# Performance work log

Measured on AMD Instinct MI355X. Metric: run time of the kernel, lower is better.

Reference implementation:

```python
import jax, jax.numpy as jnp
import numpy as np

B, S, D = 2, 2048, 2048
H = 16
HD = D // H  # head_dim = 128


def setup_inputs() -> dict:
    key = jax.random.key(0)
    ks = jax.random.split(key, 5)
    scale = 1.0 / np.sqrt(D)
    x = jax.random.normal(ks[0], (B, S, D), dtype=jnp.float32)
    Wq = jax.random.normal(ks[1], (D, D), dtype=jnp.float32) * scale
    Wk = jax.random.normal(ks[2], (D, D), dtype=jnp.float32) * scale
    Wv = jax.random.normal(ks[3], (D, D), dtype=jnp.float32) * scale
    Wo = jax.random.normal(ks[4], (D, D), dtype=jnp.float32) * scale
    bo = jnp.zeros((D,), dtype=jnp.float32)
    return {"x": x, "Wq": Wq, "Wk": Wk, "Wv": Wv, "Wo": Wo, "bo": bo}


def reference(x, Wq, Wk, Wv, Wo, bo):
    b, s, _ = x.shape
    # projections (nn.Linear: y = x @ W^T, here W stored as [in, out] already)
    q = (x @ Wq).reshape(b, s, H, HD).transpose(0, 2, 1, 3)  # [B,H,S,HD]
    k = (x @ Wk).reshape(b, s, H, HD).transpose(0, 2, 1, 3)
    v = (x @ Wv).reshape(b, s, H, HD).transpose(0, 2, 1, 3)
    scores = jnp.einsum("bhqd,bhkd->bhqk", q, k)
    causal = jnp.triu(jnp.ones((s, s), dtype=bool), k=1)
    scores = jnp.where(causal[None, None], -jnp.inf, scores)
    attn = jax.nn.softmax(scores / np.sqrt(HD), axis=-1)  # dropout=0 (eval)
    out = jnp.einsum("bhqk,bhkd->bhqd", attn, v)
    out = out.transpose(0, 2, 1, 3).reshape(b, s, D)
    return out @ Wo + bo
```

## Files before the change

### kernel.cpp

```cpp
#include <hip/hip_runtime.h>

#define S_LEN 2048
#define D_MODEL 2048
#define NH 16
#define HD 128

typedef __attribute__((ext_vector_type(4))) float f32x4;
typedef __attribute__((ext_vector_type(8))) short short8;
typedef __attribute__((ext_vector_type(8))) __bf16 bf16x8;
typedef __attribute__((ext_vector_type(4))) unsigned short us4;

__device__ __forceinline__ unsigned short f2bf(float f) {
  unsigned int u = __builtin_bit_cast(unsigned int, f);
  return (unsigned short)((u + 0x7fffu + ((u >> 16) & 1u)) >> 16);
}

__device__ __forceinline__ f32x4 mfma_bf16(short8 a, short8 b, f32x4 c) {
  return __builtin_amdgcn_mfma_f32_16x16x32_bf16(
      __builtin_bit_cast(bf16x8, a), __builtin_bit_cast(bf16x8, b), c, 0, 0, 0);
}

__device__ __forceinline__ void gload16(const unsigned short* g, unsigned short* l) {
  __builtin_amdgcn_global_load_lds(
      (const __attribute__((address_space(1))) void*)g,
      (__attribute__((address_space(3))) void*)l, 16, 0, 0);
}

__global__ void cast_bf16_2(const float* __restrict__ src, unsigned short* __restrict__ dst0,
                            unsigned short* __restrict__ dst1) {
  int i = blockIdx.x * blockDim.x + threadIdx.x;
  float4 v = ((const float4*)src)[i];
  us4 o = { f2bf(v.x), f2bf(v.y), f2bf(v.z), f2bf(v.w) };
  if (i < 1048576) ((us4*)dst0)[i] = o;
  else             ((us4*)dst1)[i - 1048576] = o;
}

__global__ void transpose_cast3(const float* __restrict__ Wq, const float* __restrict__ Wk,
                                const float* __restrict__ Wv, unsigned short* __restrict__ Wt) {
  __shared__ unsigned short tile[32][33];
  const float* W = (blockIdx.z == 0) ? Wq : (blockIdx.z == 1) ? Wk : Wv;
  unsigned short* dst = Wt + (size_t)blockIdx.z * 4194304;
  int bx = blockIdx.x * 32, by = blockIdx.y * 32;
  int tx = threadIdx.x, ty = threadIdx.y;
#pragma unroll
  for (int i = 0; i < 32; i += 8)
    tile[ty + i][tx] = f2bf(W[(by + ty + i) * D_MODEL + bx + tx]);
  __syncthreads();
#pragma unroll
  for (int i = 0; i < 32; i += 8)
    dst[(bx + ty + i) * D_MODEL + by + tx] = tile[tx][ty + i];
}

__global__ void transpose_cast(const float* __restrict__ W, unsigned short* __restrict__ Wt) {
  __shared__ unsigned short tile[32][33];
  int bx = blockIdx.x * 32, by = blockIdx.y * 32;
  int tx = threadIdx.x, ty = threadIdx.y;
#pragma unroll
  for (int i = 0; i < 32; i += 8)
    tile[ty + i][tx] = f2bf(W[(by + ty + i) * D_MODEL + bx + tx]);
  __syncthreads();
#pragma unroll
  for (int i = 0; i < 32; i += 8)
    Wt[(bx + ty + i) * D_MODEL + by + tx] = tile[tx][ty + i];
}

#define GEMM_KLOOP(Ag0, Ag1, Bg0, Bg1, acc, t, fu, wr, wc, lr)           \
  __shared__ unsigned short lA[3][128 * 32];                             \
  __shared__ unsigned short lB[3][128 * 32];                             \
  do {                                                                   \
    const int nt = D_MODEL >> 5;                                         \
    _Pragma("unroll") for (int i = 0; i < 2; i++) {                      \
      const int _k = i * 32;                                             \
      gload16(Ag0 + _k, lA[i] + t * 8);                                  \
      gload16(Ag1 + _k, lA[i] + 2048 + t * 8);                           \
      gload16(Bg0 + _k, lB[i] + t * 8);                                  \
      gload16(Bg1 + _k, lB[i] + 2048 + t * 8);                           \
    }                                                                    \
    int cur = 0;                                                         \
    for (int tk = 0; tk < nt; ++tk) {                                    \
      if (tk + 1 < nt) {                                                 \
        asm volatile("s_waitcnt vmcnt(4)" ::: "memory");                 \
      } else {                                                           \
        asm volatile("s_waitcnt vmcnt(0)" ::: "memory");                 \
      }                                                                  \
      __builtin_amdgcn_sched_barrier(0);                                 \
      __builtin_amdgcn_s_barrier();                                      \
      __builtin_amdgcn_sched_barrier(0);                                 \
      if (tk + 2 < nt) {                                                 \
        int nx2 = cur + 2;                                               \
        if (nx2 >= 3) nx2 -= 3;                                          \
        const int _k = (tk + 2) * 32;                                    \
        gload16(Ag0 + _k, lA[nx2] + t * 8);                              \
        gload16(Ag1 + _k, lA[nx2] + 2048 + t * 8);                       \
        gload16(Bg0 + _k, lB[nx2] + t * 8);                              \
        gload16(Bg1 + _k, lB[nx2] + 2048 + t * 8);                       \
      }                                                                  \
      const unsigned short* a = lA[cur];                                 \
      const unsigned short* b = lB[cur];                                 \
      short8 af[4], bf[4];                                               \
      _Pragma("unroll") for (int mi = 0; mi < 4; mi++)                   \
        af[mi] = *(const short8*)&a[(wr * 64 + mi * 16 + lr) * 32 + fu]; \
      _Pragma("unroll") for (int ni = 0; ni < 4; ni++)                   \
        bf[ni] = *(const short8*)&b[(wc * 64 + ni * 16 + lr) * 32 + fu]; \
      __builtin_amdgcn_s_setprio(1);                                     \
      _Pragma("unroll") for (int mi = 0; mi < 4; mi++)                   \
        _Pragma("unroll") for (int ni = 0; ni < 4; ni++)                 \
          acc[mi][ni] = mfma_bf16(af[mi], bf[ni], acc[mi][ni]);          \
      __builtin_amdgcn_s_setprio(0);                                     \
      cur = (cur == 2) ? 0 : cur + 1;                                    \
    }                                                                    \
  } while (0)

__global__ __launch_bounds__(256, 3) void gemm_qkv(
    const unsigned short* __restrict__ A, const unsigned short* __restrict__ Bt,
    unsigned short* __restrict__ qb, unsigned short* __restrict__ kb,
    unsigned short* __restrict__ vtb) {
  const int t = threadIdx.x;
  const int l = t & 63, w = t >> 6;
  const int wr = w >> 1, wc = w & 1;
  const int lr = l & 15, lk = l >> 4;
  const int n0 = blockIdx.x * 128, m0 = blockIdx.y * 128;

  const int arow = t >> 2;
  const int au = ((t & 3) ^ ((arow >> 1) & 3)) * 8;
  const unsigned short* Ag0 = A + (size_t)(m0 + arow) * D_MODEL + au;
  const unsigned short* Ag1 = Ag0 + 64 * D_MODEL;
  const unsigned short* Bg0 = Bt + (size_t)(n0 + arow) * D_MODEL + au;
  const unsigned short* Bg1 = Bg0 + 64 * D_MODEL;
  const int fu = (lk ^ ((lr >> 1) & 3)) * 8;

  f32x4 acc[4][4] = {};
  GEMM_KLOOP(Ag0, Ag1, Bg0, Bg1, acc, t, fu, wr, wc, lr);

  if (n0 < 4096) {
    unsigned short* C = (n0 < 2048) ? qb : kb;
    const int nbase = n0 & 2047;
#pragma unroll
    for (int mi = 0; mi < 4; mi++) {
      int r0 = m0 + wr * 64 + mi * 16 + lk * 4;
#pragma unroll
      for (int ni = 0; ni < 4; ni++) {
        int c2 = nbase + wc * 64 + ni * 16 + lr;
#pragma unroll
        for (int r = 0; r < 4; r++)
          C[(size_t)(r0 + r) * D_MODEL + c2] = f2bf(acc[mi][ni][r]);
      }
    }
  } else {
    const int nb = n0 - 4096;
#pragma unroll
    for (int mi = 0; mi < 4; mi++) {
      int s = m0 + wr * 64 + mi * 16 + lk * 4;
#pragma unroll
      for (int ni = 0; ni < 4; ni++) {
        int n = nb + wc * 64 + ni * 16 + lr;
        int h = n >> 7, d = n & (HD - 1);
        us4 pk = { f2bf(acc[mi][ni][0]), f2bf(acc[mi][ni][1]),
                   f2bf(acc[mi][ni][2]), f2bf(acc[mi][ni][3]) };
        *(us4*)&vtb[((size_t)(h * HD + d)) * S_LEN + s] = pk;
      }
    }
  }
}

__global__ __launch_bounds__(256, 3) void gemm_out(
    const unsigned short* __restrict__ ctx0, const unsigned short* __restrict__ ctx1,
    const unsigned short* __restrict__ Bt, const float* __restrict__ bias,
    float* __restrict__ out) {
  const int t = threadIdx.x;
  const int l = t & 63, w = t >> 6;
  const int wr = w >> 1, wc = w & 1;
  const int lr = l & 15, lk = l >> 4;
  const int n0 = blockIdx.x * 128, m0 = blockIdx.y * 128;

  const unsigned short* Ablk = (m0 < 2048)
      ? ctx0 + (size_t)m0 * D_MODEL
      : ctx1 + (size_t)(m0 - 2048) * D_MODEL;

  const int arow = t >> 2;
  const int au = ((t & 3) ^ ((arow >> 1) & 3)) * 8;
  const unsigned short* Ag0 = Ablk + (size_t)arow * D_MODEL + au;
  const unsigned short* Ag1 = Ag0 + 64 * D_MODEL;
  const unsigned short* Bg0 = Bt + (size_t)(n0 + arow) * D_MODEL + au;
  const unsigned short* Bg1 = Bg0 + 64 * D_MODEL;
  const int fu = (lk ^ ((lr >> 1) & 3)) * 8;

  f32x4 acc[4][4] = {};
  GEMM_KLOOP(Ag0, Ag1, Bg0, Bg1, acc, t, fu, wr, wc, lr);

#pragma unroll
  for (int mi = 0; mi < 4; mi++) {
    int r0 = m0 + wr * 64 + mi * 16 + lk * 4;
#pragma unroll
    for (int ni = 0; ni < 4; ni++) {
      int c2 = n0 + wc * 64 + ni * 16 + lr;
      float bv = bias[c2];
#pragma unroll
      for (int r = 0; r < 4; r++)
        out[(size_t)(r0 + r) * D_MODEL + c2] = acc[mi][ni][r] + bv;
    }
  }
}

__global__ __launch_bounds__(256, 2) void attn_kernel(
    const unsigned short* __restrict__ Q, const unsigned short* __restrict__ K,
    const unsigned short* __restrict__ Vt, unsigned short* __restrict__ ctx) {
  __shared__ unsigned short lds[36864];

  const int id = blockIdx.x;
  const int h = id & 15;
  const int qtl = id >> 4;
  const int qt = (qtl < 16) ? (2 * qtl) : (63 - 2 * qtl);

  const int t = threadIdx.x, l = t & 63, w = t >> 6;
  const int lr = l & 15, lk = l >> 4;

  const float qscale = 0.08838834764831845f * 1.44269504088896340f;
  const unsigned short* qsrc = Q + (size_t)(qt * 64 + w * 16 + lr) * D_MODEL + h * HD;
  short8 Qf[4];
#pragma unroll
  for (int kk = 0; kk < 4; kk++) {
    short8 qv = *(const short8*)&qsrc[kk * 32 + lk * 8];
#pragma unroll
    for (int e = 0; e < 8; e++) {
      unsigned int u = ((unsigned int)(unsigned short)qv[e]) << 16;
      float f = __builtin_bit_cast(float, u) * qscale;
      qv[e] = (short)f2bf(f);
    }
    Qf[kk] = qv;
  }

  const unsigned short* ksrc = K + h * HD;
  const unsigned short* vsrc = Vt + (size_t)h * HD * S_LEN;
  const int krow = t >> 4, kcs = t & 15;
  const int vrow = t >> 3, vcs = t & 7;

#define STAGE_KV(par, kv0base)                                                    \
  do {                                                                            \
    unsigned short* lKb = lds + (par) * 8192;                                     \
    unsigned short* lVb = lds + 16384 + (par) * 8192;                             \
    _Pragma("unroll") for (int i = 0; i < 4; i++) {                               \
      int row = i * 16 + krow;                                                    \
      gload16(ksrc + (size_t)((kv0base) + row) * D_MODEL + ((kcs ^ (row & 7)) * 8), \
              lKb + row * 128 + kcs * 8);                                         \
    }                                                                             \
    _Pragma("unroll") for (int i = 0; i < 4; i++) {                               \
      int row = i * 32 + vrow;                                                    \
      gload16(vsrc + (size_t)row * S_LEN + (kv0base) + ((vcs ^ (row & 7)) * 8),   \
              lVb + row * 64 + vcs * 8);                                          \
    }                                                                             \
  } while (0)

  f32x4 O[8] = {};
  float l_s = 0.f;
  const float M0 = 8.0f;
  const int nkv = qt + 1;
  unsigned short* lPw = lds + 32768 + w * 1024;

  STAGE_KV(0, 0);

  for (int tk = 0; tk < nkv; tk++) {
    const int kv0 = tk * 64;
    const int par = tk & 1;
    const unsigned short* lKc = lds + par * 8192;
    const unsigned short* lVc = lds + 16384 + par * 8192;

    asm volatile("s_waitcnt vmcnt(0)" ::: "memory");
    __builtin_amdgcn_sched_barrier(0);
    __builtin_amdgcn_s_barrier();
    __builtin_amdgcn_sched_barrier(0);

    if (tk + 1 < nkv) STAGE_KV(par ^ 1, kv0 + 64);

    f32x4 sc[4] = {};
    __builtin_amdgcn_s_setprio(1);
#pragma unroll
    for (int kk = 0; kk < 4; kk++) {
      short8 Kf[4];
#pragma unroll
      for (int ni = 0; ni < 4; ni++)
        Kf[ni] = *(const short8*)&lKc[(ni * 16 + lr) * 128 + (((kk * 4 + lk) ^ (lr & 7)) * 8)];
#pragma unroll
      for (int ni = 0; ni < 4; ni++)
        sc[ni] = mfma_bf16(Kf[ni], Qf[kk], sc[ni]);
    }
    __builtin_amdgcn_s_setprio(0);

    const int row0g = qt * 64 + w * 16 + lr;
    if (tk == qt) {
#pragma unroll
      for (int ni = 0; ni < 4; ni++) {
        const int colb = kv0 + ni * 16 + lk * 4;
#pragma unroll
        for (int r = 0; r < 4; r++)
          if (colb + r > row0g) sc[ni][r] = -1e30f;
      }
    }

    float rs = 0.f;
#pragma unroll
    for (int ni = 0; ni < 4; ni++)
#pragma unroll
      for (int r = 0; r < 4; r++) {
        float p = __builtin_amdgcn_exp2f(sc[ni][r] - M0);
        sc[ni][r] = p;
        rs += p;
      }
    rs += __shfl_xor(rs, 16);
    rs += __shfl_xor(rs, 32);
    l_s += rs;

#pragma unroll
    for (int ni = 0; ni < 4; ni++) {
      us4 pk = { f2bf(sc[ni][0]), f2bf(sc[ni][1]), f2bf(sc[ni][2]), f2bf(sc[ni][3]) };
      int u16 = (ni * 2 + (lk >> 1)) ^ (lr & 7);
      *(us4*)&lPw[lr * 64 + u16 * 8 + (lk & 1) * 4] = pk;
    }

    __builtin_amdgcn_s_setprio(1);
#pragma unroll
    for (int kk = 0; kk < 2; kk++) {
      short8 Pf = *(const short8*)&lPw[lr * 64 + (((kk * 4 + lk) ^ (lr & 7)) * 8)];
#pragma unroll
      for (int di = 0; di < 8; di++) {
        short8 Vf = *(const short8*)&lVc[(di * 16 + lr) * 64 + (((kk * 4 + lk) ^ (lr & 7)) * 8)];
        O[di] = mfma_bf16(Pf, Vf, O[di]);
      }
    }
    __builtin_amdgcn_s_setprio(0);
  }
#undef STAGE_KV

  float lr4[4];
#pragma unroll
  for (int r = 0; r < 4; r++) lr4[r] = __shfl(l_s, lk * 4 + r);
#pragma unroll
  for (int di = 0; di < 8; di++)
#pragma unroll
    for (int r = 0; r < 4; r++) {
      float v = O[di][r] / lr4[r];
      ctx[(size_t)(qt * 64 + w * 16 + lk * 4 + r) * D_MODEL + h * HD + di * 16 + lr] = f2bf(v);
    }
}

extern "C" void kernel_launch(void* const* d_in, const int* in_sizes, int n_in,
                              void* d_out, int out_size, void* d_ws, size_t ws_size,
                              hipStream_t stream) {
  const float* x  = (const float*)d_in[0];
  const float* Wq = (const float*)d_in[1];
  const float* Wk = (const float*)d_in[2];
  const float* Wv = (const float*)d_in[3];
  const float* Wo = (const float*)d_in[4];
  const float* bo = (const float*)d_in[5];
  float* out = (float*)d_out;

  unsigned short* ws = (unsigned short*)d_ws;
  unsigned short* S0 = ws;
  unsigned short* S1 = ws + 1 * 4194304;
  unsigned short* S2 = ws + 2 * 4194304;
  unsigned short* S3 = ws + 3 * 4194304;
  unsigned short* S4 = ws + 4 * 4194304;
  unsigned short* wqkvt = (unsigned short*)d_out;
  unsigned short* xb1   = wqkvt + 12582912;

  dim3 tb(32, 8);

  transpose_cast3<<<dim3(64, 64, 3), tb, 0, stream>>>(Wq, Wk, Wv, wqkvt);
  cast_bf16_2<<<8192, 256, 0, stream>>>(x, S0, xb1);

  for (int b = 0; b < 2; b++) {
    const unsigned short* xb = (b == 0) ? S0 : xb1;
    unsigned short* ctx = (b == 0) ? S4 : S0;

    gemm_qkv<<<dim3(48, 16), 256, 0, stream>>>(xb, wqkvt, S1, S2, S3);
    attn_kernel<<<dim3(512), 256, 0, stream>>>(S1, S2, S3, ctx);
  }

  transpose_cast<<<dim3(64, 64), tb, 0, stream>>>(Wo, S1);
  gemm_out<<<dim3(16, 32), 256, 0, stream>>>(S4, S0, S1, bo, out);
}
```

Before: 284.5 us.

## Rewrite QKV GEMM as 256x256-tile 8-wave kernel with interleaved staging

Replaces the 128x128-tile, 4-wave QKV projection GEMM with a 256x256-tile, 512-thread kernel. It uses double-buffered LDS with 64-wide K steps and a hand-scheduled sequence of barriers that interleaves global-to-LDS loads with quarter-tile MFMA groups. The larger tile raises arithmetic intensity and cuts redundant global traffic. In exchange the grid shrinks to 192 blocks per batch, fewer than the CU count, and LDS use per block rises to about 128 KB, which limits occupancy to one block per CU.

```diff
diff --git a/kernel.cpp b/kernel.cpp
--- a/kernel.cpp
+++ b/kernel.cpp
@@ -62,6 +62,150 @@
 #pragma unroll
   for (int i = 0; i < 32; i += 8)
     Wt[(bx + ty + i) * D_MODEL + by + tx] = tile[tx][ty + i];
+}
+
+__global__ __launch_bounds__(512, 2) void gemm_qkv(
+    const unsigned short* __restrict__ A, const unsigned short* __restrict__ Bt,
+    unsigned short* __restrict__ qb, unsigned short* __restrict__ kb,
+    unsigned short* __restrict__ vtb) {
+  __shared__ unsigned short lA[2][16384];
+  __shared__ unsigned short lB[2][16384];
+  const int t = threadIdx.x;
+  const int l = t & 63, w = t >> 6;
+  const int wm = w >> 2, wn = w & 3;
+  const int lr = l & 15, lk = l >> 4;
+  const int n0 = blockIdx.x * 256, m0 = blockIdx.y * 256;
+
+  const int t8 = t * 8;
+  const int srow = t >> 3;
+  const int gu8 = ((t & 7) ^ ((t >> 3) & 7)) * 8;
+  const unsigned short* asrc = A + (size_t)(m0 + srow) * D_MODEL + gu8;
+  const unsigned short* bsrc = Bt + (size_t)(n0 + srow) * D_MODEL + gu8;
+
+  const int aBase = (wm * 128 + lr) * 64;
+  const int bBase = (wn * 64 + lr) * 64;
+  const int aoff0 = (lk ^ (lr & 7)) * 8;
+  const int aoff1 = ((4 + lk) ^ (lr & 7)) * 8;
+
+  f32x4 acc[8][4] = {};
+  short8 af[4][2], bf[4][2];
+
+#define STG_A8(buf, koff, j) gload16(asrc + (size_t)(j) * 131072 + (koff), lA[buf] + (j) * 4096 + t8)
+#define STG_B8(buf, koff, j) gload16(bsrc + (size_t)(j) * 131072 + (koff), lB[buf] + (j) * 4096 + t8)
+#define RDA(p, mi0)                                                          \
+  _Pragma("unroll") for (int m = 0; m < 4; m++) {                            \
+    af[m][0] = *(const short8*)&lA[p][aBase + ((mi0) + m) * 1024 + aoff0];   \
+    af[m][1] = *(const short8*)&lA[p][aBase + ((mi0) + m) * 1024 + aoff1];   \
+  }
+#define RDB(p, ni0)                                                          \
+  _Pragma("unroll") for (int n = 0; n < 2; n++) {                            \
+    bf[(ni0) + n][0] = *(const short8*)&lB[p][bBase + ((ni0) + n) * 1024 + aoff0]; \
+    bf[(ni0) + n][1] = *(const short8*)&lB[p][bBase + ((ni0) + n) * 1024 + aoff1]; \
+  }
+#define MM16(mi0, ni0)                                                       \
+  __builtin_amdgcn_s_setprio(1);                                             \
+  _Pragma("unroll") for (int m = 0; m < 4; m++)                              \
+  _Pragma("unroll") for (int n = 0; n < 2; n++) {                            \
+    acc[(mi0)+m][(ni0)+n] = mfma_bf16(af[m][0], bf[(ni0)+n][0], acc[(mi0)+m][(ni0)+n]); \
+    acc[(mi0)+m][(ni0)+n] = mfma_bf16(af[m][1], bf[(ni0)+n][1], acc[(mi0)+m][(ni0)+n]); \
+  }                                                                          \
+  __builtin_amdgcn_s_setprio(0);
+#define BARRIER asm volatile("s_barrier" ::: "memory")
+#define SCHED0 __builtin_amdgcn_sched_barrier(0)
+
+#pragma unroll
+  for (int j = 0; j < 4; j++) STG_A8(0, 0, j);
+#pragma unroll
+  for (int j = 0; j < 4; j++) STG_B8(0, 0, j);
+  STG_A8(1, 64, 0); STG_A8(1, 64, 1);
+  asm volatile("s_waitcnt vmcnt(2)" ::: "memory");
+  BARRIER;
+
+#pragma unroll 1
+  for (int i = 0; i < 16; ++i) {
+    const bool more = (i < 15);
+    const size_t o1 = (size_t)(2 * i + 1) * 64;
+    const size_t o2 = (size_t)(2 * i + 2) * 64;
+    const size_t o3 = (size_t)(2 * i + 3) * 64;
+    RDA(0, 0); RDB(0, 0);
+    STG_A8(1, o1, 2); STG_A8(1, o1, 3);
+    BARRIER; SCHED0;
+    MM16(0, 0);
+    BARRIER;
+    RDB(0, 2);
+    STG_B8(1, o1, 0); STG_B8(1, o1, 1);
+    BARRIER; SCHED0;
+    MM16(0, 2);
+    BARRIER;
+    RDA(0, 4);
+    STG_B8(1, o1, 2); STG_B8(1, o1, 3);
+    BARRIER; SCHED0;
+    MM16(4, 2);
+    BARRIER;
+    if (more) { STG_A8(0, o2, 0); STG_A8(0, o2, 1); }
+    BARRIER; SCHED0;
+    MM16(4, 0);
+    if (more) { asm volatile("s_waitcnt vmcnt(2)" ::: "memory"); }
+    else      { asm volatile("s_waitcnt vmcnt(0)" ::: "memory"); }
+    BARRIER;
+    RDA(1, 0); RDB(1, 0);
+    if (more) { STG_A8(0, o2, 2); STG_A8(0, o2, 3); }
+    BARRIER; SCHED0;
+    MM16(0, 0);
+    BARRIER;
+    RDB(1, 2);
+    if (more) { STG_B8(0, o2, 0); STG_B8(0, o2, 1); }
+    BARRIER; SCHED0;
+    MM16(0, 2);
+    BARRIER;
+    RDA(1, 4);
+    if (more) { STG_B8(0, o2, 2); STG_B8(0, o2, 3); }
+    BARRIER; SCHED0;
+    MM16(4, 2);
+    BARRIER;
+    if (more) { STG_A8(1, o3, 0); STG_A8(1, o3, 1); }
+    BARRIER; SCHED0;
+    MM16(4, 0);
+    if (more) { asm volatile("s_waitcnt vmcnt(2)" ::: "memory"); }
+    BARRIER;
+  }
+#undef STG_A8
+#undef STG_B8
+#undef RDA
+#undef RDB
+#undef MM16
+#undef BARRIER
+#undef SCHED0
+
+  if (n0 < 4096) {
+    unsigned short* C = (n0 < 2048) ? qb : kb;
+    const int nbase = n0 & 2047;
+#pragma unroll
+    for (int mi = 0; mi < 8; mi++) {
+      int r0 = m0 + wm * 128 + mi * 16 + lk * 4;
+#pragma unroll
+      for (int ni = 0; ni < 4; ni++) {
+        int c2 = nbase + wn * 64 + ni * 16 + lr;
+#pragma unroll
+        for (int r = 0; r < 4; r++)
+          C[(size_t)(r0 + r) * D_MODEL + c2] = f2bf(acc[mi][ni][r]);
+      }
+    }
+  } else {
+    const int nb0 = n0 - 4096;
+#pragma unroll
+    for (int mi = 0; mi < 8; mi++) {
+      int s = m0 + wm * 128 + mi * 16 + lk * 4;
+#pragma unroll
+      for (int ni = 0; ni < 4; ni++) {
+        int n = nb0 + wn * 64 + ni * 16 + lr;
+        int h = n >> 7, d = n & (HD - 1);
+        us4 pk = { f2bf(acc[mi][ni][0]), f2bf(acc[mi][ni][1]),
+                   f2bf(acc[mi][ni][2]), f2bf(acc[mi][ni][3]) };
+        *(us4*)&vtb[((size_t)(h * HD + d)) * S_LEN + s] = pk;
+      }
+    }
+  }
 }
 
 #define GEMM_KLOOP(Ag0, Ag1, Bg0, Bg1, acc, t, fu, wr, wc, lr)           \
@@ -111,58 +255,6 @@
     }                                                                    \
   } while (0)
 
-__global__ __launch_bounds__(256, 3) void gemm_qkv(
-    const unsigned short* __restrict__ A, const unsigned short* __restrict__ Bt,
-    unsigned short* __restrict__ qb, unsigned short* __restrict__ kb,
-    unsigned short* __restrict__ vtb) {
-  const int t = threadIdx.x;
-  const int l = t & 63, w = t >> 6;
-  const int wr = w >> 1, wc = w & 1;
-  const int lr = l & 15, lk = l >> 4;
-  const int n0 = blockIdx.x * 128, m0 = blockIdx.y * 128;
-
-  const int arow = t >> 2;
-  const int au = ((t & 3) ^ ((arow >> 1) & 3)) * 8;
-  const unsigned short* Ag0 = A + (size_t)(m0 + arow) * D_MODEL + au;
-  const unsigned short* Ag1 = Ag0 + 64 * D_MODEL;
-  const unsigned short* Bg0 = Bt + (size_t)(n0 + arow) * D_MODEL + au;
-  const unsigned short* Bg1 = Bg0 + 64 * D_MODEL;
-  const int fu = (lk ^ ((lr >> 1) & 3)) * 8;
-
-  f32x4 acc[4][4] = {};
-  GEMM_KLOOP(Ag0, Ag1, Bg0, Bg1, acc, t, fu, wr, wc, lr);
-
-  if (n0 < 4096) {
-    unsigned short* C = (n0 < 2048) ? qb : kb;
-    const int nbase = n0 & 2047;
-#pragma unroll
-    for (int mi = 0; mi < 4; mi++) {
-      int r0 = m0 + wr * 64 + mi * 16 + lk * 4;
-#pragma unroll
-      for (int ni = 0; ni < 4; ni++) {
-        int c2 = nbase + wc * 64 + ni * 16 + lr;
-#pragma unroll
-        for (int r = 0; r < 4; r++)
-          C[(size_t)(r0 + r) * D_MODEL + c2] = f2bf(acc[mi][ni][r]);
-      }
-    }
-  } else {
-    const int nb = n0 - 4096;
-#pragma unroll
-    for (int mi = 0; mi < 4; mi++) {
-      int s = m0 + wr * 64 + mi * 16 + lk * 4;
-#pragma unroll
-      for (int ni = 0; ni < 4; ni++) {
-        int n = nb + wc * 64 + ni * 16 + lr;
-        int h = n >> 7, d = n & (HD - 1);
-        us4 pk = { f2bf(acc[mi][ni][0]), f2bf(acc[mi][ni][1]),
-                   f2bf(acc[mi][ni][2]), f2bf(acc[mi][ni][3]) };
-        *(us4*)&vtb[((size_t)(h * HD + d)) * S_LEN + s] = pk;
-      }
-    }
-  }
-}
-
 __global__ __launch_bounds__(256, 3) void gemm_out(
     const unsigned short* __restrict__ ctx0, const unsigned short* __restrict__ ctx1,
     const unsigned short* __restrict__ Bt, const float* __restrict__ bias,
@@ -372,7 +464,7 @@
     const unsigned short* xb = (b == 0) ? S0 : xb1;
     unsigned short* ctx = (b == 0) ? S4 : S0;
 
-    gemm_qkv<<<dim3(48, 16), 256, 0, stream>>>(xb, wqkvt, S1, S2, S3);
+    gemm_qkv<<<dim3(24, 8), 512, 0, stream>>>(xb, wqkvt, S1, S2, S3);
     attn_kernel<<<dim3(512), 256, 0, stream>>>(S1, S2, S3, ctx);
   }
 
```

Result: no change. 289.8 us (+1.9%).

## Rewrite attention to load K/V directly into registers with split-KV waves

Applied to the files above, without the earlier changes.

The attention kernel drops LDS staging of K/V tiles and the per-wave P round-trip through shared memory. Each wave now loads 16-row K and V fragments straight from global memory into registers, double-buffered. The four waves split as two query groups by two interleaved KV halves, and the halves are merged through LDS at the end. P stays in registers and feeds a 16x16x16 MFMA, and the GEMM launch bounds occupancy hint drops from 3 to 2. This removes barriers and LDS traffic per KV tile, at the cost of uncoalesced global loads without cross-wave reuse, higher register pressure, and a final reduction step.

```diff
diff --git a/kernel.cpp b/kernel.cpp
--- a/kernel.cpp
+++ b/kernel.cpp
@@ -7,6 +7,7 @@
 
 typedef __attribute__((ext_vector_type(4))) float f32x4;
 typedef __attribute__((ext_vector_type(8))) short short8;
+typedef __attribute__((ext_vector_type(4))) short s16x4;
 typedef __attribute__((ext_vector_type(8))) __bf16 bf16x8;
 typedef __attribute__((ext_vector_type(4))) unsigned short us4;
 
@@ -18,6 +19,15 @@
 __device__ __forceinline__ f32x4 mfma_bf16(short8 a, short8 b, f32x4 c) {
   return __builtin_amdgcn_mfma_f32_16x16x32_bf16(
       __builtin_bit_cast(bf16x8, a), __builtin_bit_cast(bf16x8, b), c, 0, 0, 0);
+}
+
+__device__ __forceinline__ f32x4 mfma16_bf16(s16x4 a, s16x4 b, f32x4 c) {
+#if __has_builtin(__builtin_amdgcn_mfma_f32_16x16x16bf16_1k)
+  return __builtin_amdgcn_mfma_f32_16x16x16bf16_1k(a, b, c, 0, 0, 0);
+#else
+  asm("v_mfma_f32_16x16x16_bf16 %0, %1, %2, %0" : "+v"(c) : "v"(a), "v"(b));
+  return c;
+#endif
 }
 
 __device__ __forceinline__ void gload16(const unsigned short* g, unsigned short* l) {
@@ -111,7 +121,7 @@
     }                                                                    \
   } while (0)
 
-__global__ __launch_bounds__(256, 3) void gemm_qkv(
+__global__ __launch_bounds__(256, 2) void gemm_qkv(
     const unsigned short* __restrict__ A, const unsigned short* __restrict__ Bt,
     unsigned short* __restrict__ qb, unsigned short* __restrict__ kb,
     unsigned short* __restrict__ vtb) {
@@ -163,7 +173,7 @@
   }
 }
 
-__global__ __launch_bounds__(256, 3) void gemm_out(
+__global__ __launch_bounds__(256, 2) void gemm_out(
     const unsigned short* __restrict__ ctx0, const unsigned short* __restrict__ ctx1,
     const unsigned short* __restrict__ Bt, const float* __restrict__ bias,
     float* __restrict__ out) {
@@ -205,7 +215,8 @@
 __global__ __launch_bounds__(256, 2) void attn_kernel(
     const unsigned short* __restrict__ Q, const unsigned short* __restrict__ K,
     const unsigned short* __restrict__ Vt, unsigned short* __restrict__ ctx) {
-  __shared__ unsigned short lds[36864];
+  __shared__ float eO[2][16][64][4];
+  __shared__ float eL[2][2][16];
 
   const int id = blockIdx.x;
   const int h = id & 15;
@@ -213,134 +224,112 @@
   const int qt = (qtl < 16) ? (2 * qtl) : (63 - 2 * qtl);
 
   const int t = threadIdx.x, l = t & 63, w = t >> 6;
+  const int wq = w >> 1, wk = w & 1;
   const int lr = l & 15, lk = l >> 4;
+  const int qgb = qt * 64 + wq * 32;
 
   const float qscale = 0.08838834764831845f * 1.44269504088896340f;
-  const unsigned short* qsrc = Q + (size_t)(qt * 64 + w * 16 + lr) * D_MODEL + h * HD;
-  short8 Qf[4];
-#pragma unroll
-  for (int kk = 0; kk < 4; kk++) {
-    short8 qv = *(const short8*)&qsrc[kk * 32 + lk * 8];
-#pragma unroll
-    for (int e = 0; e < 8; e++) {
-      unsigned int u = ((unsigned int)(unsigned short)qv[e]) << 16;
-      float f = __builtin_bit_cast(float, u) * qscale;
-      qv[e] = (short)f2bf(f);
-    }
-    Qf[kk] = qv;
-  }
-
-  const unsigned short* ksrc = K + h * HD;
-  const unsigned short* vsrc = Vt + (size_t)h * HD * S_LEN;
-  const int krow = t >> 4, kcs = t & 15;
-  const int vrow = t >> 3, vcs = t & 7;
-
-#define STAGE_KV(par, kv0base)                                                    \
-  do {                                                                            \
-    unsigned short* lKb = lds + (par) * 8192;                                     \
-    unsigned short* lVb = lds + 16384 + (par) * 8192;                             \
-    _Pragma("unroll") for (int i = 0; i < 4; i++) {                               \
-      int row = i * 16 + krow;                                                    \
-      gload16(ksrc + (size_t)((kv0base) + row) * D_MODEL + ((kcs ^ (row & 7)) * 8), \
-              lKb + row * 128 + kcs * 8);                                         \
-    }                                                                             \
-    _Pragma("unroll") for (int i = 0; i < 4; i++) {                               \
-      int row = i * 32 + vrow;                                                    \
-      gload16(vsrc + (size_t)row * S_LEN + (kv0base) + ((vcs ^ (row & 7)) * 8),   \
-              lVb + row * 64 + vcs * 8);                                          \
-    }                                                                             \
+  short8 Qf[2][4];
+#pragma unroll
+  for (int qc = 0; qc < 2; qc++)
+#pragma unroll
+    for (int kk = 0; kk < 4; kk++) {
+      short8 qv = *(const short8*)&Q[(size_t)(qgb + qc * 16 + lr) * D_MODEL + h * HD + kk * 32 + lk * 8];
+#pragma unroll
+      for (int e = 0; e < 8; e++) {
+        unsigned int u = ((unsigned int)(unsigned short)qv[e]) << 16;
+        float f = __builtin_bit_cast(float, u) * qscale;
+        qv[e] = (short)f2bf(f);
+      }
+      Qf[qc][kk] = qv;
+    }
+
+  const unsigned short* kbase = K + h * HD;
+  const unsigned short* vbase = Vt + (size_t)h * HD * S_LEN;
+
+  const int nkv16 = qt * 4 + 2 + 2 * wq;
+  const int nt = (nkv16 - wk + 1) >> 1;
+
+  f32x4 O0[8] = {}, O1[8] = {};
+  float ls0 = 0.f, ls1 = 0.f;
+  short8 KA[4], KB[4];
+  s16x4 VA[8], VB[8];
+
+#define LOADKV(KX, VX, j_)                                                          \
+  do {                                                                              \
+    const int kv0_ = (wk + 2 * (j_)) * 16;                                          \
+    _Pragma("unroll") for (int kk = 0; kk < 4; kk++)                                \
+      KX[kk] = *(const short8*)&kbase[(size_t)(kv0_ + lr) * D_MODEL + kk * 32 + lk * 8]; \
+    _Pragma("unroll") for (int dt = 0; dt < 8; dt++)                                \
+      VX[dt] = *(const s16x4*)&vbase[(size_t)(dt * 16 + lr) * S_LEN + kv0_ + lk * 4];    \
   } while (0)
 
-  f32x4 O[8] = {};
-  float l_s = 0.f;
-  const float M0 = 8.0f;
-  const int nkv = qt + 1;
-  unsigned short* lPw = lds + 32768 + w * 1024;
-
-  STAGE_KV(0, 0);
-
-  for (int tk = 0; tk < nkv; tk++) {
-    const int kv0 = tk * 64;
-    const int par = tk & 1;
-    const unsigned short* lKc = lds + par * 8192;
-    const unsigned short* lVc = lds + 16384 + par * 8192;
-
-    asm volatile("s_waitcnt vmcnt(0)" ::: "memory");
-    __builtin_amdgcn_sched_barrier(0);
-    __builtin_amdgcn_s_barrier();
-    __builtin_amdgcn_sched_barrier(0);
-
-    if (tk + 1 < nkv) STAGE_KV(par ^ 1, kv0 + 64);
-
-    f32x4 sc[4] = {};
-    __builtin_amdgcn_s_setprio(1);
-#pragma unroll
-    for (int kk = 0; kk < 4; kk++) {
-      short8 Kf[4];
-#pragma unroll
-      for (int ni = 0; ni < 4; ni++)
-        Kf[ni] = *(const short8*)&lKc[(ni * 16 + lr) * 128 + (((kk * 4 + lk) ^ (lr & 7)) * 8)];
-#pragma unroll
-      for (int ni = 0; ni < 4; ni++)
-        sc[ni] = mfma_bf16(Kf[ni], Qf[kk], sc[ni]);
-    }
-    __builtin_amdgcn_s_setprio(0);
-
-    const int row0g = qt * 64 + w * 16 + lr;
-    if (tk == qt) {
-#pragma unroll
-      for (int ni = 0; ni < 4; ni++) {
-        const int colb = kv0 + ni * 16 + lk * 4;
-#pragma unroll
-        for (int r = 0; r < 4; r++)
-          if (colb + r > row0g) sc[ni][r] = -1e30f;
-      }
-    }
-
-    float rs = 0.f;
-#pragma unroll
-    for (int ni = 0; ni < 4; ni++)
-#pragma unroll
-      for (int r = 0; r < 4; r++) {
-        float p = __builtin_amdgcn_exp2f(sc[ni][r] - M0);
-        sc[ni][r] = p;
-        rs += p;
-      }
-    rs += __shfl_xor(rs, 16);
-    rs += __shfl_xor(rs, 32);
-    l_s += rs;
-
-#pragma unroll
-    for (int ni = 0; ni < 4; ni++) {
-      us4 pk = { f2bf(sc[ni][0]), f2bf(sc[ni][1]), f2bf(sc[ni][2]), f2bf(sc[ni][3]) };
-      int u16 = (ni * 2 + (lk >> 1)) ^ (lr & 7);
-      *(us4*)&lPw[lr * 64 + u16 * 8 + (lk & 1) * 4] = pk;
-    }
-
-    __builtin_amdgcn_s_setprio(1);
-#pragma unroll
-    for (int kk = 0; kk < 2; kk++) {
-      short8 Pf = *(const short8*)&lPw[lr * 64 + (((kk * 4 + lk) ^ (lr & 7)) * 8)];
-#pragma unroll
-      for (int di = 0; di < 8; di++) {
-        short8 Vf = *(const short8*)&lVc[(di * 16 + lr) * 64 + (((kk * 4 + lk) ^ (lr & 7)) * 8)];
-        O[di] = mfma_bf16(Pf, Vf, O[di]);
-      }
-    }
-    __builtin_amdgcn_s_setprio(0);
-  }
-#undef STAGE_KV
-
-  float lr4[4];
-#pragma unroll
-  for (int r = 0; r < 4; r++) lr4[r] = __shfl(l_s, lk * 4 + r);
-#pragma unroll
-  for (int di = 0; di < 8; di++)
-#pragma unroll
-    for (int r = 0; r < 4; r++) {
-      float v = O[di][r] / lr4[r];
-      ctx[(size_t)(qt * 64 + w * 16 + lk * 4 + r) * D_MODEL + h * HD + di * 16 + lr] = f2bf(v);
-    }
+#define COMPUTE(KX, VX, j_)                                                         \
+  do {                                                                              \
+    const int kv0_ = (wk + 2 * (j_)) * 16;                                          \
+    f32x4 sc0 = {}, sc1 = {};                                                       \
+    _Pragma("unroll") for (int kk = 0; kk < 4; kk++) {                              \
+      sc0 = mfma_bf16(KX[kk], Qf[0][kk], sc0);                                      \
+      sc1 = mfma_bf16(KX[kk], Qf[1][kk], sc1);                                      \
+    }                                                                               \
+    if (kv0_ + 15 > qgb) {                                                          \
+      _Pragma("unroll") for (int r = 0; r < 4; r++) {                               \
+        const int kg = kv0_ + lk * 4 + r;                                           \
+        if (kg > qgb + lr) sc0[r] = -1e30f;                                         \
+        if (kg > qgb + 16 + lr) sc1[r] = -1e30f;                                    \
+      }                                                                             \
+    }                                                                               \
+    _Pragma("unroll") for (int r = 0; r < 4; r++) {                                 \
+      float p0 = __builtin_amdgcn_exp2f(sc0[r] - 8.0f);                             \
+      float p1 = __builtin_amdgcn_exp2f(sc1[r] - 8.0f);                             \
+      sc0[r] = p0; sc1[r] = p1; ls0 += p0; ls1 += p1;                               \
+    }                                                                               \
+    s16x4 P0 = { (short)f2bf(sc0[0]), (short)f2bf(sc0[1]),                          \
+                 (short)f2bf(sc0[2]), (short)f2bf(sc0[3]) };                        \
+    s16x4 P1 = { (short)f2bf(sc1[0]), (short)f2bf(sc1[1]),                          \
+                 (short)f2bf(sc1[2]), (short)f2bf(sc1[3]) };                        \
+    _Pragma("unroll") for (int dt = 0; dt < 8; dt++) {                              \
+      O0[dt] = mfma16_bf16(VX[dt], P0, O0[dt]);                                     \
+      O1[dt] = mfma16_bf16(VX[dt], P1, O1[dt]);                                     \
+    }                                                                               \
+  } while (0)
+
+  if (nt > 0) LOADKV(KA, VA, 0);
+  for (int j = 0; j < nt; j += 2) {
+    if (j + 1 < nt) LOADKV(KB, VB, j + 1);
+    COMPUTE(KA, VA, j);
+    if (j + 2 < nt) LOADKV(KA, VA, j + 2);
+    if (j + 1 < nt) COMPUTE(KB, VB, j + 1);
+  }
+#undef LOADKV
+#undef COMPUTE
+
+  ls0 += __shfl_xor(ls0, 16); ls0 += __shfl_xor(ls0, 32);
+  ls1 += __shfl_xor(ls1, 16); ls1 += __shfl_xor(ls1, 32);
+
+  __syncthreads();
+  if (wk == 1) {
+#pragma unroll
+    for (int dt = 0; dt < 8; dt++) {
+      *(f32x4*)&eO[wq][dt][l][0] = O0[dt];
+      *(f32x4*)&eO[wq][8 + dt][l][0] = O1[dt];
+    }
+    if (lk == 0) { eL[wq][0][lr] = ls0; eL[wq][1][lr] = ls1; }
+  }
+  __syncthreads();
+  if (wk == 0) {
+    const float inv0 = 1.0f / (ls0 + eL[wq][0][lr]);
+    const float inv1 = 1.0f / (ls1 + eL[wq][1][lr]);
+#pragma unroll
+    for (int dt = 0; dt < 8; dt++) {
+      f32x4 o0 = O0[dt] + *(const f32x4*)&eO[wq][dt][l][0];
+      f32x4 o1 = O1[dt] + *(const f32x4*)&eO[wq][8 + dt][l][0];
+      us4 s0 = { f2bf(o0[0] * inv0), f2bf(o0[1] * inv0), f2bf(o0[2] * inv0), f2bf(o0[3] * inv0) };
+      us4 s1 = { f2bf(o1[0] * inv1), f2bf(o1[1] * inv1), f2bf(o1[2] * inv1), f2bf(o1[3] * inv1) };
+      *(us4*)&ctx[(size_t)(qgb + lr) * D_MODEL + h * HD + dt * 16 + lk * 4] = s0;
+      *(us4*)&ctx[(size_t)(qgb + 16 + lr) * D_MODEL + h * HD + dt * 16 + lk * 4] = s1;
+    }
+  }
 }
 
 extern "C" void kernel_launch(void* const* d_in, const int* in_sizes, int n_in,
```

After: 378.5 us. 33.1% more time.
